# Optimization experiments

Measured on AMD Instinct MI355X. Metric: run time of the kernel, lower is better.

Reference implementation:

```python
import jax, jax.numpy as jnp
import numpy as np

EMBED_DIM = 1024
Q_HEADS = 16
KV_HEADS = 8            # n_heads // 2 per CrossAttention
HEAD_DIM = EMBED_DIM // Q_HEADS   # 64
KV_EMBED = HEAD_DIM * KV_HEADS    # 512
GROUPS = Q_HEADS // KV_HEADS      # 2
LN_EPS = 1e-5
RMS_EPS = 1e-6


def _rms_norm(x):
    # SimpleRMSNorm (no learned scale) used inside BitLinear
    return x * jax.lax.rsqrt(jnp.mean(jnp.square(x), axis=-1, keepdims=True) + RMS_EPS)


def _act_quant(x):
    # per-token 8-bit absmax activation quant (BitNet b1.58)
    scale = 127.0 / jnp.maximum(jnp.max(jnp.abs(x), axis=-1, keepdims=True), 1e-5)
    return jnp.clip(jnp.round(x * scale), -128.0, 127.0) / scale


def _weight_quant(w):
    # ternary {-1,0,1} absmean weight quant
    scale = 1.0 / jnp.maximum(jnp.mean(jnp.abs(w)), 1e-5)
    return jnp.clip(jnp.round(w * scale), -1.0, 1.0) / scale


def _ste(a, q):
    # straight-through estimator: forward=q, backward=identity
    return a + jax.lax.stop_gradient(q - a)


def bit_linear(x, w):
    # x: [b, n, in], w: [out, in] (torch Linear layout), no bias
    xn = _rms_norm(x)
    xq = _ste(xn, _act_quant(xn))
    wq = _ste(w, _weight_quant(w))
    return jnp.einsum('bni,oi->bno', xq, wq)


def setup_inputs() -> dict:
    key = jax.random.key(0)
    ks = jax.random.split(key, 6)
    B, N, S, D = 16, 1024, 256, EMBED_DIM
    s = D ** -0.5
    return {
        'x': jax.random.normal(ks[0], (B, N, D), jnp.float32),
        'y': jax.random.normal(ks[1], (B, S, D), jnp.float32),
        'wq': jax.random.normal(ks[2], (D, D), jnp.float32) * s,
        'wk': jax.random.normal(ks[3], (KV_EMBED, D), jnp.float32) * s,
        'wv': jax.random.normal(ks[4], (KV_EMBED, D), jnp.float32) * s,
        'wo': jax.random.normal(ks[5], (D, D), jnp.float32) * s,
        'ln_gamma': jnp.ones((D,), jnp.float32),
        'ln_beta': jnp.zeros((D,), jnp.float32),
    }


def reference(x, y, wq, wk, wv, wo, ln_gamma, ln_beta):
    B, N, D = x.shape
    S = y.shape[1]
    # ternary-quantized projections
    q = bit_linear(x, wq).reshape(B, N, Q_HEADS, HEAD_DIM)
    k = bit_linear(y, wk).reshape(B, S, KV_HEADS, HEAD_DIM)
    v = bit_linear(y, wv).reshape(B, S, KV_HEADS, HEAD_DIM)
    # grouped-query attention: split q heads as (kv_head, group)
    q = jnp.transpose(q, (0, 2, 1, 3)) / (HEAD_DIM ** 0.5)   # [b, Hq, n, d]
    q = q.reshape(B, KV_HEADS, GROUPS, N, HEAD_DIM)           # [b, h, g, n, d]
    k = jnp.transpose(k, (0, 2, 1, 3))                        # [b, h, s, d]
    v = jnp.transpose(v, (0, 2, 1, 3))
    scores = jnp.einsum('bhgnd,bhsd->bhgns', q, k)
    attn = jax.nn.softmax(scores, axis=-1)                    # is_causal=False, no mask
    out = jnp.einsum('bhgns,bhsd->bhgnd', attn, v)
    out = jnp.transpose(out, (0, 3, 1, 2, 4)).reshape(B, N, D)  # b n (h g) d -> b n D
    # LayerNorm before out projection
    mu = jnp.mean(out, axis=-1, keepdims=True)
    var = jnp.mean(jnp.square(out - mu), axis=-1, keepdims=True)
    out = (out - mu) * jax.lax.rsqrt(var + LN_EPS) * ln_gamma + ln_beta
    return bit_linear(out, wo)
```

## Files before the change

### kernel.cpp

```cpp
#include <hip/hip_runtime.h>
#include <hip/hip_bf16.h>

typedef int int4v __attribute__((ext_vector_type(4)));
typedef float float4v __attribute__((ext_vector_type(4)));
typedef _Float16 half8 __attribute__((ext_vector_type(8)));

#define DEV __device__ __forceinline__

DEV signed char quant8(float v) {
    int q = (int)rintf(v);
    q = q < -128 ? -128 : (q > 127 ? 127 : q);
    return (signed char)q;
}

DEV int tern1(float v) {
    int q = (int)rintf(v);
    q = q < -1 ? -1 : (q > 1 ? 1 : q);
    return q;
}

DEV void gl2lds16(const void* g, void* l) {
    __builtin_amdgcn_global_load_lds(
        (const __attribute__((address_space(1))) void*)g,
        (__attribute__((address_space(3))) void*)l, 16, 0, 0);
}

__global__ __launch_bounds__(256) void absmean_all(
    const float* __restrict__ WQ, const float* __restrict__ WK,
    const float* __restrict__ WV, const float* __restrict__ WO,
    double* __restrict__ part)
{
    __shared__ double red[256];
    int bx = blockIdx.x, t = threadIdx.x;
    const float* W; int rel;
    if (bx < 64)       { W = WQ; rel = bx; }
    else if (bx < 96)  { W = WK; rel = bx - 64; }
    else if (bx < 128) { W = WV; rel = bx - 96; }
    else               { W = WO; rel = bx - 128; }
    size_t base = (size_t)rel * 16384;
    double acc = 0.0;
    for (int i = t; i < 16384; i += 256) acc += (double)fabsf(W[base + i]);
    red[t] = acc; __syncthreads();
    #pragma unroll
    for (int o = 128; o > 0; o >>= 1) {
        if (t < o) red[t] += red[t + o];
        __syncthreads();
    }
    if (t == 0) part[bx] = red[0];
}

__global__ __launch_bounds__(256) void betas_kernel(
    const double* __restrict__ part, float* __restrict__ betas)
{
    int t = threadIdx.x, w = t >> 6, lane = t & 63;
    const int offs[4]   = {0, 64, 96, 128};
    const int cnts[4]   = {64, 32, 32, 64};
    const int counts[4] = {1048576, 524288, 524288, 1048576};
    double v = (lane < cnts[w]) ? part[offs[w] + lane] : 0.0;
    #pragma unroll
    for (int o = 32; o > 0; o >>= 1) v += __shfl_down(v, o);
    if (lane == 0) betas[w] = fmaxf((float)(v / (double)counts[w]), 1e-5f);
}

__global__ __launch_bounds__(256) void wquant_all(
    const float* __restrict__ WQ, const float* __restrict__ WK,
    const float* __restrict__ WV, const float* __restrict__ WO,
    signed char* __restrict__ w8, const float* __restrict__ betas)
{
    int bx = blockIdx.x;
    const float* W; signed char* O; float inv; int rel;
    if (bx < 1024)      { W = WQ; O = w8;                           rel = bx;        inv = 1.f / betas[0]; }
    else if (bx < 1536) { W = WK; O = w8 + (1 << 20);               rel = bx - 1024; inv = 1.f / betas[1]; }
    else if (bx < 2048) { W = WV; O = w8 + (1 << 20) + (512 << 10); rel = bx - 1536; inv = 1.f / betas[2]; }
    else                { W = WO; O = w8 + (2 << 20);               rel = bx - 2048; inv = 1.f / betas[3]; }
    int i = rel * 256 + threadIdx.x;
    float4 u = ((const float4*)W)[i];
    int q0 = tern1(u.x * inv);
    int q1 = tern1(u.y * inv);
    int q2 = tern1(u.z * inv);
    int q3 = tern1(u.w * inv);
    int packed = (q0 & 0xff) | ((q1 & 0xff) << 8) | ((q2 & 0xff) << 16) | ((q3 & 0xff) << 24);
    ((int*)O)[i] = packed;
}

__global__ __launch_bounds__(256) void act_quant(
    const float* __restrict__ X, signed char* __restrict__ X8,
    float* __restrict__ RS)
{
    int row = blockIdx.x * 4 + (threadIdx.x >> 6);
    int lane = threadIdx.x & 63;
    const float4* xr = (const float4*)(X + (size_t)row * 1024) + lane * 4;
    float4 u[4];
    #pragma unroll
    for (int i = 0; i < 4; i++) u[i] = xr[i];
    float ss = 0.f, am = 0.f;
    #pragma unroll
    for (int i = 0; i < 4; i++) {
        ss += u[i].x * u[i].x + u[i].y * u[i].y + u[i].z * u[i].z + u[i].w * u[i].w;
        am = fmaxf(am, fmaxf(fmaxf(fabsf(u[i].x), fabsf(u[i].y)),
                             fmaxf(fabsf(u[i].z), fabsf(u[i].w))));
    }
    #pragma unroll
    for (int o = 32; o > 0; o >>= 1) {
        ss += __shfl_xor(ss, o);
        am = fmaxf(am, __shfl_xor(am, o));
    }
    float r = 1.f / sqrtf(ss * (1.f / 1024.f) + 1e-6f);
    float m = fmaxf(am * r, 1e-5f);
    float s = 127.f / m;
    int pk[4];
    #pragma unroll
    for (int i = 0; i < 4; i++) {
        int q0 = quant8((u[i].x * r) * s);
        int q1 = quant8((u[i].y * r) * s);
        int q2 = quant8((u[i].z * r) * s);
        int q3 = quant8((u[i].w * r) * s);
        pk[i] = (q0 & 0xff) | ((q1 & 0xff) << 8) | ((q2 & 0xff) << 16) | ((q3 & 0xff) << 24);
    }
    int4v pv = {pk[0], pk[1], pk[2], pk[3]};
    ((int4v*)(X8 + (size_t)row * 1024))[lane] = pv;
    if (lane == 0) RS[row] = m * (1.f / 127.f);
}

__global__ __launch_bounds__(256) void gemm_i8(
    const signed char* __restrict__ A, const signed char* __restrict__ B,
    float* __restrict__ outF, _Float16* __restrict__ outH,
    _Float16* __restrict__ outK, _Float16* __restrict__ outV,
    int N, int K,
    const float* __restrict__ rowscale, const float* __restrict__ betas,
    int b0i, int b1i, int split, float extra, int mode)
{
    __shared__ __align__(16) signed char As0[128 * 64];
    __shared__ __align__(16) signed char Bs0[128 * 64];
    __shared__ __align__(16) signed char As1[128 * 64];
    __shared__ __align__(16) signed char Bs1[128 * 64];
    const int tid = threadIdx.x;
    const int lane = tid & 63, wid = tid >> 6;
    const int wr = wid >> 1, wc = wid & 1;
    const int lr = lane & 15, quad = lane >> 4;

    const int flat = blockIdx.y * 8 + blockIdx.x;
    const int chunk = (gridDim.x * gridDim.y) >> 3;
    const int f2 = (flat & 7) * chunk + (flat >> 3);
    const int bM = f2 >> 3, bN = f2 & 7;

    int4v zero = {0, 0, 0, 0};
    int4v acc[4][4];
    #pragma unroll
    for (int i = 0; i < 4; i++)
        #pragma unroll
        for (int j = 0; j < 4; j++) acc[i][j] = zero;

    const int srow = wid * 32 + (lane >> 2);
    const int soff = (lane & 3) * 16;
    const signed char* gA0 = A + (size_t)(bM * 128 + srow) * K + soff;
    const signed char* gA1 = gA0 + (size_t)16 * K;
    const signed char* gB0 = B + (size_t)(bN * 128 + srow) * K + soff;
    const signed char* gB1 = gB0 + (size_t)16 * K;
    const int lo0 = wid * 2048, lo1 = wid * 2048 + 1024;

    gl2lds16(gA0, As0 + lo0);
    gl2lds16(gA1, As0 + lo1);
    gl2lds16(gB0, Bs0 + lo0);
    gl2lds16(gB1, Bs0 + lo1);
    __syncthreads();

#define GEMM_COMPUTE(AS, BS)                                                   \
    {                                                                          \
        int4v af[4], bfr[4];                                                   \
        _Pragma("unroll")                                                      \
        for (int tm = 0; tm < 4; tm++)                                         \
            af[tm] = *(const int4v*)((AS) + (wr * 64 + tm * 16 + lr) * 64 + quad * 16); \
        _Pragma("unroll")                                                      \
        for (int tn = 0; tn < 4; tn++)                                         \
            bfr[tn] = *(const int4v*)((BS) + (wc * 64 + tn * 16 + lr) * 64 + quad * 16); \
        _Pragma("unroll")                                                      \
        for (int tm = 0; tm < 4; tm++)                                         \
            _Pragma("unroll")                                                  \
            for (int tn = 0; tn < 4; tn++)                                     \
                acc[tm][tn] = __builtin_amdgcn_mfma_i32_16x16x64_i8(af[tm], bfr[tn], acc[tm][tn], 0, 0, 0); \
    }

    for (int kb = 0; kb < K; kb += 128) {
        if (kb + 64 < K) {
            gl2lds16(gA0 + kb + 64, As1 + lo0);
            gl2lds16(gA1 + kb + 64, As1 + lo1);
            gl2lds16(gB0 + kb + 64, Bs1 + lo0);
            gl2lds16(gB1 + kb + 64, Bs1 + lo1);
        }
        GEMM_COMPUTE(As0, Bs0);
        __syncthreads();
        if (kb + 128 < K) {
            gl2lds16(gA0 + kb + 128, As0 + lo0);
            gl2lds16(gA1 + kb + 128, As0 + lo1);
            gl2lds16(gB0 + kb + 128, Bs0 + lo0);
            gl2lds16(gB1 + kb + 128, Bs0 + lo1);
        }
        GEMM_COMPUTE(As1, Bs1);
        __syncthreads();
    }
#undef GEMM_COMPUTE

    const float s0 = betas[b0i] * extra, s1 = betas[b1i] * extra;
    #pragma unroll
    for (int tm = 0; tm < 4; tm++) {
        #pragma unroll
        for (int r = 0; r < 4; r++) {
            int grow = bM * 128 + wr * 64 + tm * 16 + quad * 4 + r;
            float rs = rowscale[grow];
            #pragma unroll
            for (int tn = 0; tn < 4; tn++) {
                int col = bN * 128 + wc * 64 + tn * 16 + lr;
                float v = (float)acc[tm][tn][r] * rs * (col < split ? s0 : s1);
                if (mode == 0) {
                    outF[(size_t)grow * N + col] = v;
                } else if (mode == 1) {
                    outH[(size_t)grow * 1024 + col] = (_Float16)v;
                } else {
                    if (col < 512)
                        outK[(size_t)grow * 512 + col] = (_Float16)v;
                    else
                        outV[((size_t)(grow >> 8) * 512 + (col - 512)) * 256 + (grow & 255)] = (_Float16)v;
                }
            }
        }
    }
}

__global__ __launch_bounds__(256, 4) void attn_mfma(
    const _Float16* Qh, const _Float16* __restrict__ Kh,
    const _Float16* __restrict__ Vt, _Float16* Oh)
{
    __shared__ __align__(16) _Float16 KVs[256 * 64];

    const int tid = threadIdx.x;
    const int lane = tid & 63;
    const int w = tid >> 6;
    const int lq = lane & 15;
    const int quad = lane >> 4;
    const int swz = (lq & 7) << 4;

    const int bx = blockIdx.x;
    const int nt = bx & 15, g = (bx >> 4) & 1, h = (bx >> 5) & 7, b = bx >> 8;
    const int rbase = b * 1024 + nt * 64 + w * 16;
    const int qcol0 = (h * 2 + g) * 64;

    half8 aq[2];
    #pragma unroll
    for (int ks = 0; ks < 2; ks++)
        aq[ks] = *(const half8*)(Qh + (size_t)(rbase + lq) * 1024 + qcol0 + ks * 32 + quad * 8);

    {
        int kb = tid >> 3;
        int c  = tid & 7;
        int rp = (kb & 3) | ((kb >> 1) & 12) | ((kb & 4) << 2);
        const _Float16* kg = Kh + (size_t)(b * 256 + kb) * 512 + h * 64 + c * 8;
        char* lb = (char*)KVs;
        #pragma unroll
        for (int j = 0; j < 8; j++) {
            int row = 32 * j + rp;
            int off = (row * 128 + c * 16) ^ ((row & 7) << 4);
            *(half8*)(lb + off) = *(const half8*)(kg + (size_t)32 * j * 512);
        }
    }
    __syncthreads();

    float4v acc[16];
    float4v zf = {0.f, 0.f, 0.f, 0.f};
    #pragma unroll
    for (int t = 0; t < 16; t++) acc[t] = zf;
    const int kc0 = (quad * 16) ^ swz;
    const int kc1 = (64 + quad * 16) ^ swz;
    #pragma unroll
    for (int t = 0; t < 16; t++) {
        const char* krow = (const char*)KVs + (t * 16 + lq) * 128;
        half8 kf0 = *(const half8*)(krow + kc0);
        acc[t] = __builtin_amdgcn_mfma_f32_16x16x32_f16(kf0, aq[0], acc[t], 0, 0, 0);
        half8 kf1 = *(const half8*)(krow + kc1);
        acc[t] = __builtin_amdgcn_mfma_f32_16x16x32_f16(kf1, aq[1], acc[t], 0, 0, 0);
    }

    float m = acc[0][0];
    #pragma unroll
    for (int t = 0; t < 16; t++) {
        #pragma unroll
        for (int r = 0; r < 4; r++) m = fmaxf(m, acc[t][r]);
    }
    m = fmaxf(m, __shfl_xor(m, 16));
    m = fmaxf(m, __shfl_xor(m, 32));
    float l = 0.f;
    #pragma unroll
    for (int t = 0; t < 16; t++) {
        #pragma unroll
        for (int r = 0; r < 4; r++) {
            float p = __expf(acc[t][r] - m);
            acc[t][r] = p;
            l += p;
        }
    }
    l += __shfl_xor(l, 16);
    l += __shfl_xor(l, 32);

    __syncthreads();

    {
        int row = tid >> 5, c = tid & 31;
        const _Float16* vg = Vt + ((size_t)b * 512 + h * 64 + row) * 256 + c * 8;
        char* lb = (char*)KVs;
        #pragma unroll
        for (int j = 0; j < 8; j++) {
            int rr = row + 8 * j;
            int off = (rr * 512 + c * 16) ^ ((rr & 7) << 4);
            *(half8*)(lb + off) = *(const half8*)(vg + (size_t)8 * j * 256);
        }
    }
    __syncthreads();

    float4v oacc[4];
    #pragma unroll
    for (int dt = 0; dt < 4; dt++) oacc[dt] = zf;
    #pragma unroll
    for (int ks = 0; ks < 8; ks++) {
        half8 pf;
        #pragma unroll
        for (int r = 0; r < 4; r++) {
            pf[r]     = (_Float16)acc[2 * ks][r];
            pf[4 + r] = (_Float16)acc[2 * ks + 1][r];
        }
        const int vc = (ks * 64 + quad * 16) ^ swz;
        #pragma unroll
        for (int dt = 0; dt < 4; dt++) {
            half8 bv = *(const half8*)((const char*)KVs + (dt * 16 + lq) * 512 + vc);
            oacc[dt] = __builtin_amdgcn_mfma_f32_16x16x32_f16(pf, bv, oacc[dt], 0, 0, 0);
        }
    }

    float linv = 1.f / l;
    float invr[4];
    #pragma unroll
    for (int r = 0; r < 4; r++) invr[r] = __shfl(linv, quad * 4 + r);
    #pragma unroll
    for (int dt = 0; dt < 4; dt++) {
        #pragma unroll
        for (int r = 0; r < 4; r++) {
            Oh[(size_t)(rbase + quad * 4 + r) * 1024 + qcol0 + dt * 16 + lq] =
                (_Float16)(oacc[dt][r] * invr[r]);
        }
    }
}

__global__ __launch_bounds__(256) void ln_quant(
    const _Float16* __restrict__ AO, const float* __restrict__ G,
    const float* __restrict__ Bt, signed char* __restrict__ O8,
    float* __restrict__ OS)
{
    int row = blockIdx.x * 4 + (threadIdx.x >> 6);
    int lane = threadIdx.x & 63;
    const _Float16* xr = AO + (size_t)row * 1024 + lane * 16;
    half8 h0 = *(const half8*)xr;
    half8 h1 = *(const half8*)(xr + 8);
    float x[16];
    #pragma unroll
    for (int i = 0; i < 8; i++) { x[i] = (float)h0[i]; x[8 + i] = (float)h1[i]; }
    float sx = 0.f, sx2 = 0.f;
    #pragma unroll
    for (int i = 0; i < 16; i++) { sx += x[i]; sx2 += x[i] * x[i]; }
    #pragma unroll
    for (int o = 32; o > 0; o >>= 1) {
        sx += __shfl_xor(sx, o);
        sx2 += __shfl_xor(sx2, o);
    }
    float mu = sx * (1.f / 1024.f);
    float var = sx2 * (1.f / 1024.f) - mu * mu;
    float rstd = 1.f / sqrtf(var + 1e-5f);

    const float4* gp = (const float4*)(G + lane * 16);
    const float4* bp = (const float4*)(Bt + lane * 16);
    float l[16];
    #pragma unroll
    for (int i = 0; i < 4; i++) {
        float4 gv = gp[i], bv = bp[i];
        l[i * 4 + 0] = (x[i * 4 + 0] - mu) * rstd * gv.x + bv.x;
        l[i * 4 + 1] = (x[i * 4 + 1] - mu) * rstd * gv.y + bv.y;
        l[i * 4 + 2] = (x[i * 4 + 2] - mu) * rstd * gv.z + bv.z;
        l[i * 4 + 3] = (x[i * 4 + 3] - mu) * rstd * gv.w + bv.w;
    }
    float msq = 0.f, am = 0.f;
    #pragma unroll
    for (int i = 0; i < 16; i++) { msq += l[i] * l[i]; am = fmaxf(am, fabsf(l[i])); }
    #pragma unroll
    for (int o = 32; o > 0; o >>= 1) {
        msq += __shfl_xor(msq, o);
        am = fmaxf(am, __shfl_xor(am, o));
    }
    float r2 = 1.f / sqrtf(msq * (1.f / 1024.f) + 1e-6f);
    float mx = fmaxf(am * r2, 1e-5f);
    float s = 127.f / mx;
    int pk[4];
    #pragma unroll
    for (int i = 0; i < 4; i++) {
        int q0 = quant8((l[i * 4 + 0] * r2) * s);
        int q1 = quant8((l[i * 4 + 1] * r2) * s);
        int q2 = quant8((l[i * 4 + 2] * r2) * s);
        int q3 = quant8((l[i * 4 + 3] * r2) * s);
        pk[i] = (q0 & 0xff) | ((q1 & 0xff) << 8) | ((q2 & 0xff) << 16) | ((q3 & 0xff) << 24);
    }
    int4v pv = {pk[0], pk[1], pk[2], pk[3]};
    ((int4v*)(O8 + (size_t)row * 1024))[lane] = pv;
    if (lane == 0) OS[row] = mx * (1.f / 127.f);
}

extern "C" void kernel_launch(void* const* d_in, const int* in_sizes, int n_in,
                              void* d_out, int out_size, void* d_ws, size_t ws_size,
                              hipStream_t stream)
{
    const float* X  = (const float*)d_in[0];
    const float* Y  = (const float*)d_in[1];
    const float* WQ = (const float*)d_in[2];
    const float* WK = (const float*)d_in[3];
    const float* WV = (const float*)d_in[4];
    const float* WO = (const float*)d_in[5];
    const float* G  = (const float*)d_in[6];
    const float* Bt = (const float*)d_in[7];

    char* ws = (char*)d_ws;
    float*  betas = (float*)ws;
    double* part  = (double*)(ws + 256);
    char* w8  = ws + 4096;
    char* x8  = w8 + (3 << 20);
    char* y8  = x8 + (16 << 20);
    float* xs = (float*)(y8 + (4 << 20));
    float* ys = xs + 16384;
    float* os = ys + 4096;
    _Float16* qf16 = (_Float16*)(os + 16384);
    _Float16* kf16 = qf16 + (size_t)16384 * 1024;
    _Float16* vt16 = kf16 + (size_t)4096 * 512;
    char* wq8 = w8;
    char* kv8 = w8 + (1 << 20);
    char* wo8 = w8 + (2 << 20);
    char* o8  = x8;

    absmean_all<<<192, 256, 0, stream>>>(WQ, WK, WV, WO, part);
    betas_kernel<<<1, 256, 0, stream>>>(part, betas);
    wquant_all<<<3072, 256, 0, stream>>>(WQ, WK, WV, WO, (signed char*)w8, betas);

    act_quant<<<4096, 256, 0, stream>>>(X, (signed char*)x8, xs);
    act_quant<<<1024, 256, 0, stream>>>(Y, (signed char*)y8, ys);

    gemm_i8<<<dim3(8, 128), 256, 0, stream>>>(
        (signed char*)x8, (signed char*)wq8, nullptr, qf16, nullptr, nullptr,
        1024, 1024, xs, betas, 0, 0, 1024, 0.125f, 1);
    gemm_i8<<<dim3(8, 32), 256, 0, stream>>>(
        (signed char*)y8, (signed char*)kv8, nullptr, nullptr, kf16, vt16,
        1024, 1024, ys, betas, 1, 2, 512, 1.f, 2);

    attn_mfma<<<4096, 256, 0, stream>>>(qf16, kf16, vt16, qf16);

    ln_quant<<<4096, 256, 0, stream>>>(qf16, G, Bt, (signed char*)o8, os);

    gemm_i8<<<dim3(8, 128), 256, 0, stream>>>(
        (signed char*)o8, (signed char*)wo8, (float*)d_out, nullptr, nullptr, nullptr,
        1024, 1024, os, betas, 3, 3, 1024, 1.f, 0);
}
```

Measured before the change: 324.2 us.

## Load int8 GEMM fragments directly from global into registers, dropping LDS staging

```diff
diff --git a/kernel.cpp b/kernel.cpp
--- a/kernel.cpp
+++ b/kernel.cpp
@@ -17,12 +17,6 @@
     int q = (int)rintf(v);
     q = q < -1 ? -1 : (q > 1 ? 1 : q);
     return q;
-}
-
-DEV void gl2lds16(const void* g, void* l) {
-    __builtin_amdgcn_global_load_lds(
-        (const __attribute__((address_space(1))) void*)g,
-        (__attribute__((address_space(3))) void*)l, 16, 0, 0);
 }
 
 __global__ __launch_bounds__(256) void absmean_all(
@@ -122,7 +116,7 @@
     if (lane == 0) RS[row] = m * (1.f / 127.f);
 }
 
-__global__ __launch_bounds__(256) void gemm_i8(
+__global__ __launch_bounds__(256, 3) void gemm_i8(
     const signed char* __restrict__ A, const signed char* __restrict__ B,
     float* __restrict__ outF, _Float16* __restrict__ outH,
     _Float16* __restrict__ outK, _Float16* __restrict__ outV,
@@ -130,10 +124,6 @@
     const float* __restrict__ rowscale, const float* __restrict__ betas,
     int b0i, int b1i, int split, float extra, int mode)
 {
-    __shared__ __align__(16) signed char As0[128 * 64];
-    __shared__ __align__(16) signed char Bs0[128 * 64];
-    __shared__ __align__(16) signed char As1[128 * 64];
-    __shared__ __align__(16) signed char Bs1[128 * 64];
     const int tid = threadIdx.x;
     const int lane = tid & 63, wid = tid >> 6;
     const int wr = wid >> 1, wc = wid & 1;
@@ -151,55 +141,40 @@
         #pragma unroll
         for (int j = 0; j < 4; j++) acc[i][j] = zero;
 
-    const int srow = wid * 32 + (lane >> 2);
-    const int soff = (lane & 3) * 16;
-    const signed char* gA0 = A + (size_t)(bM * 128 + srow) * K + soff;
-    const signed char* gA1 = gA0 + (size_t)16 * K;
-    const signed char* gB0 = B + (size_t)(bN * 128 + srow) * K + soff;
-    const signed char* gB1 = gB0 + (size_t)16 * K;
-    const int lo0 = wid * 2048, lo1 = wid * 2048 + 1024;
-
-    gl2lds16(gA0, As0 + lo0);
-    gl2lds16(gA1, As0 + lo1);
-    gl2lds16(gB0, Bs0 + lo0);
-    gl2lds16(gB1, Bs0 + lo1);
-    __syncthreads();
-
-#define GEMM_COMPUTE(AS, BS)                                                   \
-    {                                                                          \
-        int4v af[4], bfr[4];                                                   \
+    const signed char* aB = A + (size_t)(bM * 128 + wr * 64 + lr) * K + quad * 16;
+    const signed char* bB = B + (size_t)(bN * 128 + wc * 64 + lr) * K + quad * 16;
+
+    int4v afA[4], bfA[4], afB[4], bfB[4];
+
+#define LOAD_SET(AF, BF, kb)                                                   \
+    do {                                                                       \
         _Pragma("unroll")                                                      \
         for (int tm = 0; tm < 4; tm++)                                         \
-            af[tm] = *(const int4v*)((AS) + (wr * 64 + tm * 16 + lr) * 64 + quad * 16); \
+            AF[tm] = *(const int4v*)(aB + (size_t)(tm * 16) * K + (kb));       \
         _Pragma("unroll")                                                      \
         for (int tn = 0; tn < 4; tn++)                                         \
-            bfr[tn] = *(const int4v*)((BS) + (wc * 64 + tn * 16 + lr) * 64 + quad * 16); \
+            BF[tn] = *(const int4v*)(bB + (size_t)(tn * 16) * K + (kb));       \
+    } while (0)
+
+#define MFMA_SET(AF, BF)                                                       \
+    do {                                                                       \
         _Pragma("unroll")                                                      \
         for (int tm = 0; tm < 4; tm++)                                         \
             _Pragma("unroll")                                                  \
             for (int tn = 0; tn < 4; tn++)                                     \
-                acc[tm][tn] = __builtin_amdgcn_mfma_i32_16x16x64_i8(af[tm], bfr[tn], acc[tm][tn], 0, 0, 0); \
-    }
-
+                acc[tm][tn] = __builtin_amdgcn_mfma_i32_16x16x64_i8(           \
+                    AF[tm], BF[tn], acc[tm][tn], 0, 0, 0);                     \
+    } while (0)
+
+    LOAD_SET(afA, bfA, 0);
     for (int kb = 0; kb < K; kb += 128) {
-        if (kb + 64 < K) {
-            gl2lds16(gA0 + kb + 64, As1 + lo0);
-            gl2lds16(gA1 + kb + 64, As1 + lo1);
-            gl2lds16(gB0 + kb + 64, Bs1 + lo0);
-            gl2lds16(gB1 + kb + 64, Bs1 + lo1);
-        }
-        GEMM_COMPUTE(As0, Bs0);
-        __syncthreads();
-        if (kb + 128 < K) {
-            gl2lds16(gA0 + kb + 128, As0 + lo0);
-            gl2lds16(gA1 + kb + 128, As0 + lo1);
-            gl2lds16(gB0 + kb + 128, Bs0 + lo0);
-            gl2lds16(gB1 + kb + 128, Bs0 + lo1);
-        }
-        GEMM_COMPUTE(As1, Bs1);
-        __syncthreads();
-    }
-#undef GEMM_COMPUTE
+        if (kb + 64 < K) LOAD_SET(afB, bfB, kb + 64);
+        MFMA_SET(afA, bfA);
+        if (kb + 128 < K) LOAD_SET(afA, bfA, kb + 128);
+        MFMA_SET(afB, bfB);
+    }
+#undef LOAD_SET
+#undef MFMA_SET
 
     const float s0 = betas[b0i] * extra, s1 = betas[b1i] * extra;
     #pragma unroll
```

Result: slower. 391.1 us (+20.6%).
